# Optimization experiments

Hardware: AMD Instinct MI355X
Metric: run time of the kernel (lower is better)

## Reference

```python
import jax, jax.numpy as jnp
import numpy as np

B, T, D = 4096, 64, 100   # trajectories, observed time points, feature dim (50 feat + 50 mask)
F = D // 2                # feature half
L = 64                    # latent_dim
NU = 64                   # n_gru_units / n_ode_units
K = 128                   # number of unique event times (integer grid 0..K-1)
DEC = 1                   # decoder output dim (volume)


def setup_inputs() -> dict:
    key = jax.random.key(0)
    ks = jax.random.split(key, 20)
    data = jax.random.normal(ks[0], (B, T, D), dtype=jnp.float32)
    # make mask half non-negative so (sum>0) masking is meaningful
    data = data.at[:, :, F:].set(jnp.abs(data[:, :, F:]))
    time_steps = jnp.sort(jax.random.randint(ks[1], (B, T), 0, K), axis=1)
    s = 0.1
    p = {}
    gi = D // 2 + L  # GRU gate input: latent + feature half
    p['Wu1'] = jax.random.normal(ks[2], (gi, NU), jnp.float32) * s
    p['bu1'] = jnp.zeros((NU,), jnp.float32)
    p['Wu2'] = jax.random.normal(ks[3], (NU, L), jnp.float32) * s
    p['bu2'] = jnp.zeros((L,), jnp.float32)
    p['Wr1'] = jax.random.normal(ks[4], (gi, NU), jnp.float32) * s
    p['br1'] = jnp.zeros((NU,), jnp.float32)
    p['Wr2'] = jax.random.normal(ks[5], (NU, L), jnp.float32) * s
    p['br2'] = jnp.zeros((L,), jnp.float32)
    p['Wn1'] = jax.random.normal(ks[6], (gi, NU), jnp.float32) * s
    p['bn1'] = jnp.zeros((NU,), jnp.float32)
    p['Wn2'] = jax.random.normal(ks[7], (NU, L), jnp.float32) * s
    p['bn2'] = jnp.zeros((L,), jnp.float32)
    # ODE func (tanh MLP), Euler-integrated one step per event interval
    p['Wo1'] = jax.random.normal(ks[8], (L, NU), jnp.float32) * s
    p['bo1'] = jnp.zeros((NU,), jnp.float32)
    p['Wo2'] = jax.random.normal(ks[9], (NU, L), jnp.float32) * s
    p['bo2'] = jnp.zeros((L,), jnp.float32)
    # decoder latent -> volume
    p['Wd'] = jax.random.normal(ks[10], (L, DEC), jnp.float32) * s
    p['bd'] = jnp.zeros((DEC,), jnp.float32)
    return {'data': data, 'time_steps': time_steps, **p}


def reference(data, time_steps,
              Wu1, bu1, Wu2, bu2,
              Wr1, br1, Wr2, br2,
              Wn1, bn1, Wn2, bn2,
              Wo1, bo1, Wo2, bo2,
              Wd, bd):
    f32 = data.dtype
    # pad one zero row at end of time axis (torch: cat(data, zeros[:,1]))
    data_pad = jnp.concatenate([data, jnp.zeros((B, 1, D), f32)], axis=1)  # [B, T+1, D]

    # presence[b, k] = 1 if event time k observed for trajectory b
    presence = jnp.zeros((B, K), f32).at[jnp.arange(B)[:, None], time_steps].set(1.0)
    upd_all = presence.T  # [K, B]  (update_mask per step)
    # fetched_count before step k = number of observed events with time < k
    counts = jnp.concatenate([jnp.zeros((B, 1), f32), jnp.cumsum(presence, axis=1)[:, :-1]], axis=1)
    idx_all = jnp.clip(counts.astype(jnp.int32), 0, T).T  # [K, B]
    rows = jnp.arange(B)

    def step(prev_y, inp):
        idx_i, upd_i = inp  # [B] int, [B] float
        upd = upd_i[:, None]
        # ODE solver: linspace gives 2 points per unit interval -> one Euler step, dt=1
        y1 = prev_y + jnp.tanh(prev_y @ Wo1 + bo1) @ Wo2 + bo2  # ode_sol end
        vol = prev_y @ Wd + bd  # decoder(ode_sol[:, :-1]) mean over single point = decoder(y0)
        fx = data_pad[rows, idx_i] * upd  # dynamic gather + mask  [B, D]
        feat, msk = fx[:, :F], fx[:, F:]
        yc = jnp.concatenate([y1, feat], axis=-1)
        u = jax.nn.sigmoid(jnp.tanh(yc @ Wu1 + bu1) @ Wu2 + bu2)
        r = jax.nn.sigmoid(jnp.tanh(yc @ Wr1 + br1) @ Wr2 + br2)
        cc = jnp.concatenate([y1 * r, feat], axis=-1)
        ns = jnp.tanh(cc @ Wn1 + bn1) @ Wn2 + bn2
        ny = (1.0 - u) * ns + u * y1
        m = (jnp.sum(msk, axis=-1, keepdims=True) > 0).astype(f32)
        ny = m * ny + (1.0 - m) * y1
        prev_y = ny * upd + y1 * (1.0 - upd)
        return prev_y, vol

    prev_y0 = jnp.zeros((B, L), f32)
    prev_y, volume_dt = jax.lax.scan(step, prev_y0, (idx_all, upd_all))
    volume_dt = jnp.transpose(volume_dt, (1, 0, 2))  # [B, K, DEC]

    # inverse_indices == time_steps values on the integer event grid
    inv = jnp.clip(time_steps[:, :-1], 0, K - 2)
    selected_state = jnp.take_along_axis(volume_dt[:, 1:], inv[:, :, None], axis=1)  # [B, T-1, DEC]
    time_intervals = (time_steps[:, 1:] - time_steps[:, :-1]).astype(f32)
    return prev_y, selected_state, time_intervals
```

## Files before the change

kernel.cpp:

```cpp
#include <hip/hip_runtime.h>


typedef __attribute__((ext_vector_type(8))) _Float16 half8;
typedef __attribute__((ext_vector_type(4))) float floatx4;

#define MFMA(a, b, c) __builtin_amdgcn_mfma_f32_16x16x32_f16((a), (b), (c), 0, 0, 0)

__device__ __forceinline__ floatx4 mfma3(half8 ah, half8 al, half8 bh, half8 bl,
                                         floatx4 c) {
    c = MFMA(ah, bh, c);
    c = MFMA(ah, bl, c);
    c = MFMA(al, bh, c);
    return c;
}

__device__ __forceinline__ float tanhf_fast(float x) {
    float e = __builtin_exp2f(x * 2.8853900817779268f);
    return 1.0f - 2.0f / (e + 1.0f);
}
__device__ __forceinline__ float sigmoidf_fast(float x) {
    float e = __builtin_exp2f(x * -1.4426950408889634f);
    return 1.0f / (1.0f + e);
}

struct W2 { half8 h, l; };

__global__ __launch_bounds__(256, 1)
void lobrm_fused(const float* __restrict__ data,
                 const int*   __restrict__ tsteps,
                 const float* __restrict__ Wu1, const float* __restrict__ bu1,
                 const float* __restrict__ Wu2, const float* __restrict__ bu2,
                 const float* __restrict__ Wr1, const float* __restrict__ br1,
                 const float* __restrict__ Wr2, const float* __restrict__ br2,
                 const float* __restrict__ Wn1, const float* __restrict__ bn1,
                 const float* __restrict__ Wn2, const float* __restrict__ bn2,
                 const float* __restrict__ Wo1, const float* __restrict__ bo1,
                 const float* __restrict__ Wo2, const float* __restrict__ bo2,
                 const float* __restrict__ Wd,  const float* __restrict__ bd,
                 float* __restrict__ out)
{
    __shared__ __align__(16) _Float16 sYh [16 * 72],  sYl [16 * 72];
    __shared__ __align__(16) _Float16 sTh [16 * 72],  sTl [16 * 72];
    __shared__ __align__(16) _Float16 sHuh[16 * 72],  sHul[16 * 72];
    __shared__ __align__(16) _Float16 sHrh[16 * 72],  sHrl[16 * 72];
    __shared__ __align__(16) _Float16 sHnh[16 * 72],  sHnl[16 * 72];
    __shared__ __align__(16) _Float16 sYCh[16 * 136], sYCl[16 * 136];
    __shared__ __align__(16) _Float16 sCCh[16 * 136], sCCl[16 * 136];
    __shared__ float    sYf[16 * 68];
    __shared__ float    sWd[64];
    __shared__ float    sVol[16 * 132];
    __shared__ unsigned sFlg[16];

    const int tid   = threadIdx.x;
    const int lane  = tid & 63;
    const int wv    = tid >> 6;
    const int col16 = lane & 15;
    const int quad  = lane >> 4;
    const int ncol  = wv * 16 + col16;
    const int rowBase = blockIdx.x * 16;

    for (int x = tid; x < 16 * 72; x += 256) { sYh[x] = (_Float16)0.f; sYl[x] = (_Float16)0.f; }
    for (int x = tid; x < 16 * 136; x += 256) {
        sYCh[x] = (_Float16)0.f; sYCl[x] = (_Float16)0.f;
        sCCh[x] = (_Float16)0.f; sCCl[x] = (_Float16)0.f;
    }
    for (int x = tid; x < 16 * 68; x += 256) sYf[x] = 0.f;
    if (tid < 64) sWd[tid] = Wd[tid];
    const float bdv = bd[0];

    auto loadW = [&](const float* W, int Kw, int kb) -> W2 {
        W2 f;
#pragma unroll
        for (int j = 0; j < 8; ++j) {
            int k = kb * 32 + quad * 8 + j;
            float v = (k < Kw) ? W[k * 64 + ncol] : 0.0f;
            _Float16 h = (_Float16)v;
            f.h[j] = h;
            f.l[j] = (_Float16)(v - (float)h);
        }
        return f;
    };
    W2 wO1[2], wO2[2], wU2[2], wR2[2], wN2[2], wU1[4], wR1[4], wN1[4];
#pragma unroll
    for (int kb = 0; kb < 2; ++kb) {
        wO1[kb] = loadW(Wo1, 64, kb);
        wO2[kb] = loadW(Wo2, 64, kb);
        wU2[kb] = loadW(Wu2, 64, kb);
        wR2[kb] = loadW(Wr2, 64, kb);
        wN2[kb] = loadW(Wn2, 64, kb);
    }
#pragma unroll
    for (int kb = 0; kb < 4; ++kb) {
        wU1[kb] = loadW(Wu1, 114, kb);
        wR1[kb] = loadW(Wr1, 114, kb);
        wN1[kb] = loadW(Wn1, 114, kb);
    }
    const float bo1v = bo1[ncol], bo2v = bo2[ncol];
    const float bu1v = bu1[ncol], bu2v = bu2[ncol];
    const float br1v = br1[ncol], br2v = br2[ncol];
    const float bn1v = bn1[ncol], bn2v = bn2[ncol];

    unsigned long long mLo[4], mHi[4];
    int cnt4[4];
#pragma unroll
    for (int r4 = 0; r4 < 4; ++r4) {
        int b = rowBase + 4 * wv + r4;
        int v = tsteps[b * 64 + lane];
        unsigned long long lo = (v < 64) ? (1ull << v) : 0ull;
        unsigned long long hi = (v >= 64) ? (1ull << (v - 64)) : 0ull;
#pragma unroll
        for (int st = 1; st < 64; st <<= 1) {
            lo |= __shfl_xor(lo, st);
            hi |= __shfl_xor(hi, st);
        }
        mLo[r4] = lo; mHi[r4] = hi; cnt4[r4] = 0;
    }
    __syncthreads();

    floatx4 pc = {0.f, 0.f, 0.f, 0.f};

    const int aOff = col16 * 72 + quad * 8;
    const int ycOff = col16 * 136 + quad * 8;

    for (int i = 0; i < 128; ++i) {
        bool hasU[4];
        float fv[4], mv[4];
#pragma unroll
        for (int r4 = 0; r4 < 4; ++r4) {
            unsigned long long mm = (i < 64) ? (mLo[r4] >> i) : (mHi[r4] >> (i - 64));
            hasU[r4] = (mm & 1ull) != 0ull;
            fv[r4] = 0.f; mv[r4] = 0.f;
            if (hasU[r4]) {
                int b = rowBase + 4 * wv + r4;
                const float* dp = data + ((size_t)b * 64 + cnt4[r4]) * 100;
                cnt4[r4]++;
                if (lane < 50) { fv[r4] = dp[lane]; mv[r4] = dp[50 + lane]; }
            }
        }

        if (wv == 0) {
            int r = lane & 15, kc = lane >> 4;
            float s = 0.f;
#pragma unroll
            for (int j = 0; j < 16; ++j) {
                int k = kc * 16 + j;
                s += sYf[r * 68 + k] * sWd[k];
            }
            s += __shfl_xor(s, 16);
            s += __shfl_xor(s, 32);
            if (lane < 16) sVol[r * 132 + i] = s + bdv;
        }

        {
            half8 a0h = *(const half8*)&sYh[aOff];
            half8 a0l = *(const half8*)&sYl[aOff];
            half8 a1h = *(const half8*)&sYh[aOff + 32];
            half8 a1l = *(const half8*)&sYl[aOff + 32];
            floatx4 acc = {0.f, 0.f, 0.f, 0.f};
            acc = mfma3(a0h, a0l, wO1[0].h, wO1[0].l, acc);
            acc = mfma3(a1h, a1l, wO1[1].h, wO1[1].l, acc);
#pragma unroll
            for (int r = 0; r < 4; ++r) {
                float t = tanhf_fast(acc[r] + bo1v);
                _Float16 h = (_Float16)t;
                int idx = (quad * 4 + r) * 72 + ncol;
                sTh[idx] = h;
                sTl[idx] = (_Float16)(t - (float)h);
            }
        }
        __syncthreads();

        floatx4 y1;
        {
            half8 a0h = *(const half8*)&sTh[aOff];
            half8 a0l = *(const half8*)&sTl[aOff];
            half8 a1h = *(const half8*)&sTh[aOff + 32];
            half8 a1l = *(const half8*)&sTl[aOff + 32];
            floatx4 acc = {0.f, 0.f, 0.f, 0.f};
            acc = mfma3(a0h, a0l, wO2[0].h, wO2[0].l, acc);
            acc = mfma3(a1h, a1l, wO2[1].h, wO2[1].l, acc);
#pragma unroll
            for (int r = 0; r < 4; ++r) {
                y1[r] = pc[r] + acc[r] + bo2v;
                _Float16 h = (_Float16)y1[r];
                int idx = (quad * 4 + r) * 136 + ncol;
                sYCh[idx] = h;
                sYCl[idx] = (_Float16)(y1[r] - (float)h);
            }
        }

#pragma unroll
        for (int r4 = 0; r4 < 4; ++r4) {
            int row = 4 * wv + r4;
            if (hasU[r4]) {
                if (lane < 50) {
                    float f = fv[r4];
                    _Float16 h = (_Float16)f;
                    _Float16 l = (_Float16)(f - (float)h);
                    int idx = row * 136 + 64 + lane;
                    sYCh[idx] = h; sYCl[idx] = l;
                    sCCh[idx] = h; sCCl[idx] = l;
                }
                float ms = mv[r4];
#pragma unroll
                for (int st = 1; st < 64; st <<= 1) ms += __shfl_xor(ms, st);
                if (lane == 0) sFlg[row] = (ms > 0.f) ? 1u : 0u;
            } else if (lane == 0) {
                sFlg[row] = 0u;
            }
        }
        __syncthreads();

        {
            floatx4 aU = {0.f, 0.f, 0.f, 0.f}, aR = {0.f, 0.f, 0.f, 0.f};
#pragma unroll
            for (int kb = 0; kb < 4; ++kb) {
                half8 ah = *(const half8*)&sYCh[ycOff + kb * 32];
                half8 al = *(const half8*)&sYCl[ycOff + kb * 32];
                aU = mfma3(ah, al, wU1[kb].h, wU1[kb].l, aU);
                aR = mfma3(ah, al, wR1[kb].h, wR1[kb].l, aR);
            }
#pragma unroll
            for (int r = 0; r < 4; ++r) {
                float tu = tanhf_fast(aU[r] + bu1v);
                float tr = tanhf_fast(aR[r] + br1v);
                int idx = (quad * 4 + r) * 72 + ncol;
                _Float16 hu = (_Float16)tu, hr = (_Float16)tr;
                sHuh[idx] = hu; sHul[idx] = (_Float16)(tu - (float)hu);
                sHrh[idx] = hr; sHrl[idx] = (_Float16)(tr - (float)hr);
            }
        }
        __syncthreads();

        floatx4 uG;
        {
            half8 a0h = *(const half8*)&sHuh[aOff];
            half8 a0l = *(const half8*)&sHul[aOff];
            half8 a1h = *(const half8*)&sHuh[aOff + 32];
            half8 a1l = *(const half8*)&sHul[aOff + 32];
            floatx4 au = {0.f, 0.f, 0.f, 0.f};
            au = mfma3(a0h, a0l, wU2[0].h, wU2[0].l, au);
            au = mfma3(a1h, a1l, wU2[1].h, wU2[1].l, au);
            half8 b0h = *(const half8*)&sHrh[aOff];
            half8 b0l = *(const half8*)&sHrl[aOff];
            half8 b1h = *(const half8*)&sHrh[aOff + 32];
            half8 b1l = *(const half8*)&sHrl[aOff + 32];
            floatx4 ar = {0.f, 0.f, 0.f, 0.f};
            ar = mfma3(b0h, b0l, wR2[0].h, wR2[0].l, ar);
            ar = mfma3(b1h, b1l, wR2[1].h, wR2[1].l, ar);
#pragma unroll
            for (int r = 0; r < 4; ++r) {
                uG[r] = sigmoidf_fast(au[r] + bu2v);
                float rg = sigmoidf_fast(ar[r] + br2v);
                float cc = y1[r] * rg;
                _Float16 h = (_Float16)cc;
                int idx = (quad * 4 + r) * 136 + ncol;
                sCCh[idx] = h;
                sCCl[idx] = (_Float16)(cc - (float)h);
            }
        }
        __syncthreads();

        {
            floatx4 aN = {0.f, 0.f, 0.f, 0.f};
#pragma unroll
            for (int kb = 0; kb < 4; ++kb) {
                half8 ah = *(const half8*)&sCCh[ycOff + kb * 32];
                half8 al = *(const half8*)&sCCl[ycOff + kb * 32];
                aN = mfma3(ah, al, wN1[kb].h, wN1[kb].l, aN);
            }
#pragma unroll
            for (int r = 0; r < 4; ++r) {
                float t = tanhf_fast(aN[r] + bn1v);
                _Float16 h = (_Float16)t;
                int idx = (quad * 4 + r) * 72 + ncol;
                sHnh[idx] = h;
                sHnl[idx] = (_Float16)(t - (float)h);
            }
        }
        __syncthreads();

        {
            half8 a0h = *(const half8*)&sHnh[aOff];
            half8 a0l = *(const half8*)&sHnl[aOff];
            half8 a1h = *(const half8*)&sHnh[aOff + 32];
            half8 a1l = *(const half8*)&sHnl[aOff + 32];
            floatx4 acc = {0.f, 0.f, 0.f, 0.f};
            acc = mfma3(a0h, a0l, wN2[0].h, wN2[0].l, acc);
            acc = mfma3(a1h, a1l, wN2[1].h, wN2[1].l, acc);
#pragma unroll
            for (int r = 0; r < 4; ++r) {
                float ns = acc[r] + bn2v;
                float ny = (1.0f - uG[r]) * ns + uG[r] * y1[r];
                unsigned ap = sFlg[quad * 4 + r];
                float nY = ap ? ny : y1[r];
                pc[r] = nY;
                int rr = quad * 4 + r;
                _Float16 h = (_Float16)nY;
                sYh[rr * 72 + ncol] = h;
                sYl[rr * 72 + ncol] = (_Float16)(nY - (float)h);
                sYf[rr * 68 + ncol] = nY;
            }
        }
        __syncthreads();
    }

#pragma unroll
    for (int r = 0; r < 4; ++r) {
        int b = rowBase + quad * 4 + r;
        out[(size_t)b * 64 + ncol] = pc[r];
    }
    float* out1 = out + (size_t)4096 * 64;
    float* out2 = out1 + (size_t)4096 * 63;
#pragma unroll
    for (int r4 = 0; r4 < 4; ++r4) {
        int row = 4 * wv + r4;
        int b = rowBase + row;
        if (lane < 63) {
            int t0 = tsteps[b * 64 + lane];
            int t1 = tsteps[b * 64 + lane + 1];
            int iv = t0 < 126 ? t0 : 126;
            out1[(size_t)b * 63 + lane] = sVol[row * 132 + iv + 1];
            out2[(size_t)b * 63 + lane] = (float)(t1 - t0);
        }
    }
}

extern "C" void kernel_launch(void* const* d_in, const int* in_sizes, int n_in,
                              void* d_out, int out_size, void* d_ws, size_t ws_size,
                              hipStream_t stream) {
    const float* data   = (const float*)d_in[0];
    const int*   tsteps = (const int*)  d_in[1];
    const float* Wu1 = (const float*)d_in[2];  const float* bu1 = (const float*)d_in[3];
    const float* Wu2 = (const float*)d_in[4];  const float* bu2 = (const float*)d_in[5];
    const float* Wr1 = (const float*)d_in[6];  const float* br1 = (const float*)d_in[7];
    const float* Wr2 = (const float*)d_in[8];  const float* br2 = (const float*)d_in[9];
    const float* Wn1 = (const float*)d_in[10]; const float* bn1 = (const float*)d_in[11];
    const float* Wn2 = (const float*)d_in[12]; const float* bn2 = (const float*)d_in[13];
    const float* Wo1 = (const float*)d_in[14]; const float* bo1 = (const float*)d_in[15];
    const float* Wo2 = (const float*)d_in[16]; const float* bo2 = (const float*)d_in[17];
    const float* Wd  = (const float*)d_in[18]; const float* bd  = (const float*)d_in[19];
    float* out = (float*)d_out;

    lobrm_fused<<<dim3(256), dim3(256), 0, stream>>>(
        data, tsteps, Wu1, bu1, Wu2, bu2, Wr1, br1, Wr2, br2,
        Wn1, bn1, Wn2, bn2, Wo1, bo1, Wo2, bo2, Wd, bd, out);
}
```

Baseline: 688.2 us.

## Split MFMA accumulation chains and compute decoder volume with MFMA

Each split-fp16 matmul's three MFMA products (hh, hl, lh) now go into separate accumulators and are summed at the end. This shortens the dependent MFMA chains so independent MFMAs can overlap. The scalar LDS-based decoder dot product in wave 0 is replaced by an MFMA against a Wd fragment held in registers, which removes the fp32 state copy in shared memory and its per-step store. The per-row data pointer is now advanced incrementally instead of recomputed from a counter. The costs are extra register pressure from more live accumulators and redundant MFMA work for the mostly-zero decoder weight columns.

```diff
diff --git a/kernel.cpp b/kernel.cpp
--- a/kernel.cpp
+++ b/kernel.cpp
@@ -5,14 +5,6 @@
 typedef __attribute__((ext_vector_type(4))) float floatx4;
 
 #define MFMA(a, b, c) __builtin_amdgcn_mfma_f32_16x16x32_f16((a), (b), (c), 0, 0, 0)
-
-__device__ __forceinline__ floatx4 mfma3(half8 ah, half8 al, half8 bh, half8 bl,
-                                         floatx4 c) {
-    c = MFMA(ah, bh, c);
-    c = MFMA(ah, bl, c);
-    c = MFMA(al, bh, c);
-    return c;
-}
 
 __device__ __forceinline__ float tanhf_fast(float x) {
     float e = __builtin_exp2f(x * 2.8853900817779268f);
@@ -46,8 +38,6 @@
     __shared__ __align__(16) _Float16 sHnh[16 * 72],  sHnl[16 * 72];
     __shared__ __align__(16) _Float16 sYCh[16 * 136], sYCl[16 * 136];
     __shared__ __align__(16) _Float16 sCCh[16 * 136], sCCl[16 * 136];
-    __shared__ float    sYf[16 * 68];
-    __shared__ float    sWd[64];
     __shared__ float    sVol[16 * 132];
     __shared__ unsigned sFlg[16];
 
@@ -59,13 +49,13 @@
     const int ncol  = wv * 16 + col16;
     const int rowBase = blockIdx.x * 16;
 
-    for (int x = tid; x < 16 * 72; x += 256) { sYh[x] = (_Float16)0.f; sYl[x] = (_Float16)0.f; }
+    for (int x = tid; x < 16 * 72; x += 256) {
+        sYh[x] = (_Float16)0.f; sYl[x] = (_Float16)0.f;
+    }
     for (int x = tid; x < 16 * 136; x += 256) {
         sYCh[x] = (_Float16)0.f; sYCl[x] = (_Float16)0.f;
         sCCh[x] = (_Float16)0.f; sCCl[x] = (_Float16)0.f;
     }
-    for (int x = tid; x < 16 * 68; x += 256) sYf[x] = 0.f;
-    if (tid < 64) sWd[tid] = Wd[tid];
     const float bdv = bd[0];
 
     auto loadW = [&](const float* W, int Kw, int kb) -> W2 {
@@ -95,13 +85,24 @@
         wR1[kb] = loadW(Wr1, 114, kb);
         wN1[kb] = loadW(Wn1, 114, kb);
     }
+    W2 vwd[2];
+#pragma unroll
+    for (int kb = 0; kb < 2; ++kb)
+#pragma unroll
+        for (int j = 0; j < 8; ++j) {
+            int k = kb * 32 + quad * 8 + j;
+            float v = (col16 == 0) ? Wd[k] : 0.0f;
+            _Float16 h = (_Float16)v;
+            vwd[kb].h[j] = h;
+            vwd[kb].l[j] = (_Float16)(v - (float)h);
+        }
     const float bo1v = bo1[ncol], bo2v = bo2[ncol];
     const float bu1v = bu1[ncol], bu2v = bu2[ncol];
     const float br1v = br1[ncol], br2v = br2[ncol];
     const float bn1v = bn1[ncol], bn2v = bn2[ncol];
 
     unsigned long long mLo[4], mHi[4];
-    int cnt4[4];
+    const float* dPtr[4];
 #pragma unroll
     for (int r4 = 0; r4 < 4; ++r4) {
         int b = rowBase + 4 * wv + r4;
@@ -113,14 +114,16 @@
             lo |= __shfl_xor(lo, st);
             hi |= __shfl_xor(hi, st);
         }
-        mLo[r4] = lo; mHi[r4] = hi; cnt4[r4] = 0;
+        mLo[r4] = lo; mHi[r4] = hi;
+        dPtr[r4] = data + (size_t)b * 6400;
     }
     __syncthreads();
 
     floatx4 pc = {0.f, 0.f, 0.f, 0.f};
-
-    const int aOff = col16 * 72 + quad * 8;
-    const int ycOff = col16 * 136 + quad * 8;
+    const floatx4 z = {0.f, 0.f, 0.f, 0.f};
+
+    const int aOff  = col16 * 72 + quad * 8;
+    const int aOffH = col16 * 136 + quad * 8;
 
     for (int i = 0; i < 128; ++i) {
         bool hasU[4];
@@ -131,24 +134,10 @@
             hasU[r4] = (mm & 1ull) != 0ull;
             fv[r4] = 0.f; mv[r4] = 0.f;
             if (hasU[r4]) {
-                int b = rowBase + 4 * wv + r4;
-                const float* dp = data + ((size_t)b * 64 + cnt4[r4]) * 100;
-                cnt4[r4]++;
+                const float* dp = dPtr[r4];
+                dPtr[r4] = dp + 100;
                 if (lane < 50) { fv[r4] = dp[lane]; mv[r4] = dp[50 + lane]; }
             }
-        }
-
-        if (wv == 0) {
-            int r = lane & 15, kc = lane >> 4;
-            float s = 0.f;
-#pragma unroll
-            for (int j = 0; j < 16; ++j) {
-                int k = kc * 16 + j;
-                s += sYf[r * 68 + k] * sWd[k];
-            }
-            s += __shfl_xor(s, 16);
-            s += __shfl_xor(s, 32);
-            if (lane < 16) sVol[r * 132 + i] = s + bdv;
         }
 
         {
@@ -156,9 +145,21 @@
             half8 a0l = *(const half8*)&sYl[aOff];
             half8 a1h = *(const half8*)&sYh[aOff + 32];
             half8 a1l = *(const half8*)&sYl[aOff + 32];
-            floatx4 acc = {0.f, 0.f, 0.f, 0.f};
-            acc = mfma3(a0h, a0l, wO1[0].h, wO1[0].l, acc);
-            acc = mfma3(a1h, a1l, wO1[1].h, wO1[1].l, acc);
+            floatx4 hh = MFMA(a1h, wO1[1].h, MFMA(a0h, wO1[0].h, z));
+            floatx4 hl = MFMA(a1h, wO1[1].l, MFMA(a0h, wO1[0].l, z));
+            floatx4 lh = MFMA(a1l, wO1[1].h, MFMA(a0l, wO1[0].h, z));
+            if (wv == 0) {
+                floatx4 vhh = MFMA(a1h, vwd[1].h, MFMA(a0h, vwd[0].h, z));
+                floatx4 vhl = MFMA(a1h, vwd[1].l, MFMA(a0h, vwd[0].l, z));
+                floatx4 vlh = MFMA(a1l, vwd[1].h, MFMA(a0l, vwd[0].h, z));
+                floatx4 v = vhh + (vhl + vlh);
+                if (col16 == 0) {
+#pragma unroll
+                    for (int r = 0; r < 4; ++r)
+                        sVol[(quad * 4 + r) * 132 + i] = v[r] + bdv;
+                }
+            }
+            floatx4 acc = hh + (hl + lh);
 #pragma unroll
             for (int r = 0; r < 4; ++r) {
                 float t = tanhf_fast(acc[r] + bo1v);
@@ -172,13 +173,14 @@
 
         floatx4 y1;
         {
-            half8 a0h = *(const half8*)&sTh[aOff];
-            half8 a0l = *(const half8*)&sTl[aOff];
-            half8 a1h = *(const half8*)&sTh[aOff + 32];
-            half8 a1l = *(const half8*)&sTl[aOff + 32];
-            floatx4 acc = {0.f, 0.f, 0.f, 0.f};
-            acc = mfma3(a0h, a0l, wO2[0].h, wO2[0].l, acc);
-            acc = mfma3(a1h, a1l, wO2[1].h, wO2[1].l, acc);
+            half8 t0h = *(const half8*)&sTh[aOff];
+            half8 t0l = *(const half8*)&sTl[aOff];
+            half8 t1h = *(const half8*)&sTh[aOff + 32];
+            half8 t1l = *(const half8*)&sTl[aOff + 32];
+            floatx4 hh = MFMA(t1h, wO2[1].h, MFMA(t0h, wO2[0].h, z));
+            floatx4 hl = MFMA(t1h, wO2[1].l, MFMA(t0h, wO2[0].l, z));
+            floatx4 lh = MFMA(t1l, wO2[1].h, MFMA(t0l, wO2[0].h, z));
+            floatx4 acc = hh + (hl + lh);
 #pragma unroll
             for (int r = 0; r < 4; ++r) {
                 y1[r] = pc[r] + acc[r] + bo2v;
@@ -212,14 +214,28 @@
         __syncthreads();
 
         {
-            floatx4 aU = {0.f, 0.f, 0.f, 0.f}, aR = {0.f, 0.f, 0.f, 0.f};
-#pragma unroll
-            for (int kb = 0; kb < 4; ++kb) {
-                half8 ah = *(const half8*)&sYCh[ycOff + kb * 32];
-                half8 al = *(const half8*)&sYCl[ycOff + kb * 32];
-                aU = mfma3(ah, al, wU1[kb].h, wU1[kb].l, aU);
-                aR = mfma3(ah, al, wR1[kb].h, wR1[kb].l, aR);
-            }
+            half8 ah0 = *(const half8*)&sYCh[aOffH];
+            half8 ah1 = *(const half8*)&sYCh[aOffH + 32];
+            half8 ah2 = *(const half8*)&sYCh[aOffH + 64];
+            half8 ah3 = *(const half8*)&sYCh[aOffH + 96];
+            half8 al0 = *(const half8*)&sYCl[aOffH];
+            half8 al1 = *(const half8*)&sYCl[aOffH + 32];
+            half8 al2 = *(const half8*)&sYCl[aOffH + 64];
+            half8 al3 = *(const half8*)&sYCl[aOffH + 96];
+            floatx4 uhh = MFMA(ah3, wU1[3].h, MFMA(ah2, wU1[2].h,
+                          MFMA(ah1, wU1[1].h, MFMA(ah0, wU1[0].h, z))));
+            floatx4 uhl = MFMA(ah3, wU1[3].l, MFMA(ah2, wU1[2].l,
+                          MFMA(ah1, wU1[1].l, MFMA(ah0, wU1[0].l, z))));
+            floatx4 ulh = MFMA(al3, wU1[3].h, MFMA(al2, wU1[2].h,
+                          MFMA(al1, wU1[1].h, MFMA(al0, wU1[0].h, z))));
+            floatx4 rhh = MFMA(ah3, wR1[3].h, MFMA(ah2, wR1[2].h,
+                          MFMA(ah1, wR1[1].h, MFMA(ah0, wR1[0].h, z))));
+            floatx4 rhl = MFMA(ah3, wR1[3].l, MFMA(ah2, wR1[2].l,
+                          MFMA(ah1, wR1[1].l, MFMA(ah0, wR1[0].l, z))));
+            floatx4 rlh = MFMA(al3, wR1[3].h, MFMA(al2, wR1[2].h,
+                          MFMA(al1, wR1[1].h, MFMA(al0, wR1[0].h, z))));
+            floatx4 aU = uhh + (uhl + ulh);
+            floatx4 aR = rhh + (rhl + rlh);
 #pragma unroll
             for (int r = 0; r < 4; ++r) {
                 float tu = tanhf_fast(aU[r] + bu1v);
@@ -234,20 +250,20 @@
 
         floatx4 uG;
         {
-            half8 a0h = *(const half8*)&sHuh[aOff];
-            half8 a0l = *(const half8*)&sHul[aOff];
-            half8 a1h = *(const half8*)&sHuh[aOff + 32];
-            half8 a1l = *(const half8*)&sHul[aOff + 32];
-            floatx4 au = {0.f, 0.f, 0.f, 0.f};
-            au = mfma3(a0h, a0l, wU2[0].h, wU2[0].l, au);
-            au = mfma3(a1h, a1l, wU2[1].h, wU2[1].l, au);
-            half8 b0h = *(const half8*)&sHrh[aOff];
-            half8 b0l = *(const half8*)&sHrl[aOff];
-            half8 b1h = *(const half8*)&sHrh[aOff + 32];
-            half8 b1l = *(const half8*)&sHrl[aOff + 32];
-            floatx4 ar = {0.f, 0.f, 0.f, 0.f};
-            ar = mfma3(b0h, b0l, wR2[0].h, wR2[0].l, ar);
-            ar = mfma3(b1h, b1l, wR2[1].h, wR2[1].l, ar);
+            half8 u0h = *(const half8*)&sHuh[aOff];
+            half8 u0l = *(const half8*)&sHul[aOff];
+            half8 u1h = *(const half8*)&sHuh[aOff + 32];
+            half8 u1l = *(const half8*)&sHul[aOff + 32];
+            floatx4 au = MFMA(u1h, wU2[1].h, MFMA(u0h, wU2[0].h, z))
+                       + (MFMA(u1h, wU2[1].l, MFMA(u0h, wU2[0].l, z))
+                        + MFMA(u1l, wU2[1].h, MFMA(u0l, wU2[0].h, z)));
+            half8 r0h = *(const half8*)&sHrh[aOff];
+            half8 r0l = *(const half8*)&sHrl[aOff];
+            half8 r1h = *(const half8*)&sHrh[aOff + 32];
+            half8 r1l = *(const half8*)&sHrl[aOff + 32];
+            floatx4 ar = MFMA(r1h, wR2[1].h, MFMA(r0h, wR2[0].h, z))
+                       + (MFMA(r1h, wR2[1].l, MFMA(r0h, wR2[0].l, z))
+                        + MFMA(r1l, wR2[1].h, MFMA(r0l, wR2[0].h, z)));
 #pragma unroll
             for (int r = 0; r < 4; ++r) {
                 uG[r] = sigmoidf_fast(au[r] + bu2v);
@@ -262,13 +278,21 @@
         __syncthreads();
 
         {
-            floatx4 aN = {0.f, 0.f, 0.f, 0.f};
-#pragma unroll
-            for (int kb = 0; kb < 4; ++kb) {
-                half8 ah = *(const half8*)&sCCh[ycOff + kb * 32];
-                half8 al = *(const half8*)&sCCl[ycOff + kb * 32];
-                aN = mfma3(ah, al, wN1[kb].h, wN1[kb].l, aN);
-            }
+            half8 ah0 = *(const half8*)&sCCh[aOffH];
+            half8 ah1 = *(const half8*)&sCCh[aOffH + 32];
+            half8 ah2 = *(const half8*)&sCCh[aOffH + 64];
+            half8 ah3 = *(const half8*)&sCCh[aOffH + 96];
+            half8 al0 = *(const half8*)&sCCl[aOffH];
+            half8 al1 = *(const half8*)&sCCl[aOffH + 32];
+            half8 al2 = *(const half8*)&sCCl[aOffH + 64];
+            half8 al3 = *(const half8*)&sCCl[aOffH + 96];
+            floatx4 nhh = MFMA(ah3, wN1[3].h, MFMA(ah2, wN1[2].h,
+                          MFMA(ah1, wN1[1].h, MFMA(ah0, wN1[0].h, z))));
+            floatx4 nhl = MFMA(ah3, wN1[3].l, MFMA(ah2, wN1[2].l,
+                          MFMA(ah1, wN1[1].l, MFMA(ah0, wN1[0].l, z))));
+            floatx4 nlh = MFMA(al3, wN1[3].h, MFMA(al2, wN1[2].h,
+                          MFMA(al1, wN1[1].h, MFMA(al0, wN1[0].h, z))));
+            floatx4 aN = nhh + (nhl + nlh);
 #pragma unroll
             for (int r = 0; r < 4; ++r) {
                 float t = tanhf_fast(aN[r] + bn1v);
@@ -281,13 +305,13 @@
         __syncthreads();
 
         {
-            half8 a0h = *(const half8*)&sHnh[aOff];
-            half8 a0l = *(const half8*)&sHnl[aOff];
-            half8 a1h = *(const half8*)&sHnh[aOff + 32];
-            half8 a1l = *(const half8*)&sHnl[aOff + 32];
-            floatx4 acc = {0.f, 0.f, 0.f, 0.f};
-            acc = mfma3(a0h, a0l, wN2[0].h, wN2[0].l, acc);
-            acc = mfma3(a1h, a1l, wN2[1].h, wN2[1].l, acc);
+            half8 n0h = *(const half8*)&sHnh[aOff];
+            half8 n0l = *(const half8*)&sHnl[aOff];
+            half8 n1h = *(const half8*)&sHnh[aOff + 32];
+            half8 n1l = *(const half8*)&sHnl[aOff + 32];
+            floatx4 acc = MFMA(n1h, wN2[1].h, MFMA(n0h, wN2[0].h, z))
+                        + (MFMA(n1h, wN2[1].l, MFMA(n0h, wN2[0].l, z))
+                         + MFMA(n1l, wN2[1].h, MFMA(n0l, wN2[0].h, z)));
 #pragma unroll
             for (int r = 0; r < 4; ++r) {
                 float ns = acc[r] + bn2v;
@@ -299,7 +323,6 @@
                 _Float16 h = (_Float16)nY;
                 sYh[rr * 72 + ncol] = h;
                 sYl[rr * 72 + ncol] = (_Float16)(nY - (float)h);
-                sYf[rr * 68 + ncol] = nY;
             }
         }
         __syncthreads();
```

Result: no change. 676.4 us (-1.7%).
